# Performance work log

Measured on AMD Instinct MI355X. Metric: run time of the kernel, lower is better.

The kernel has to match this reference:

```python
import jax, jax.numpy as jnp
import numpy as np

V = 5023      # CoMA mesh vertices
K = 8         # avg neighbors per vertex
E = V * K     # edges
B = 64        # batch
C_IN = 3      # xyz
C_HID = 64    # conv width (layer_info)
M = 9         # kernel_size: number of weight matrices
LATENT = 128


def fsc_conv(x, src, dst, aw, u, c, W, b):
    """Feature-steered graph conv (translation invariant: v = -u).
    x: [B,V,C]; edge e: (i=src[e], j=dst[e]) with adjacency weight aw[e].
    y_i = b + sum_j a_ij * sum_m softmax_m(u_m.(x_i-x_j)+c_m) * (x_j @ W_m)
    """
    Bx, Vx, C = x.shape
    D = W.shape[2]
    xi = x[:, src]                                  # [B,E,C]
    xj = x[:, dst]                                  # [B,E,C]
    logits = jnp.einsum('bec,cm->bem', xi - xj, u) + c   # [B,E,M]
    att = jax.nn.softmax(logits, axis=-1) * aw[None, :, None]
    y = jnp.zeros((Bx, Vx, D), x.dtype)
    for m in range(W.shape[0]):                     # small fixed loop over M
        agg = jnp.zeros((Bx, Vx, C), x.dtype).at[:, src].add(att[:, :, m:m + 1] * xj)
        y = y + agg @ W[m]
    return y + b


def setup_inputs() -> dict:
    key = jax.random.key(0)
    ks = jax.random.split(key, 16)
    x = jax.random.normal(ks[0], (B, V, C_IN), jnp.float32)
    # mesh-like adjacency: each vertex i has K random neighbors, weight 1/K
    src = jnp.repeat(jnp.arange(V, dtype=jnp.int32), K)
    dst = jax.random.randint(ks[1], (E,), 0, V, dtype=jnp.int32)
    aw = jnp.full((E,), 1.0 / K, jnp.float32)
    g = lambda k, shp, fan: jax.random.normal(k, shp, jnp.float32) * np.float32(np.sqrt(2.0 / fan))
    # encoder conv params
    u_e = g(ks[2], (C_IN, M), C_IN + M)
    c_e = jnp.zeros((M,), jnp.float32)
    W_e = g(ks[3], (M, C_IN, C_HID), C_IN + C_HID)
    b_e = jnp.zeros((C_HID,), jnp.float32)
    # encoder latent dense: [V*C_HID, LATENT]
    W_enc = g(ks[4], (V * C_HID, LATENT), V * C_HID)
    b_enc = jnp.zeros((LATENT,), jnp.float32)
    # decoder latent dense: [LATENT, C_HID*V]
    W_dec = g(ks[5], (LATENT, C_HID * V), LATENT)
    b_dec = jnp.zeros((C_HID * V,), jnp.float32)
    # decoder conv params
    u_d = g(ks[6], (C_HID, M), C_HID + M)
    c_d = jnp.zeros((M,), jnp.float32)
    W_d = g(ks[7], (M, C_HID, C_IN), C_HID + C_IN)
    b_d = jnp.zeros((C_IN,), jnp.float32)
    return {'x': x, 'aw': aw, 'u_e': u_e, 'c_e': c_e, 'W_e': W_e, 'b_e': b_e,
            'W_enc': W_enc, 'b_enc': b_enc, 'W_dec': W_dec, 'b_dec': b_dec,
            'u_d': u_d, 'c_d': c_d, 'W_d': W_d, 'b_d': b_d,
            'src': src, 'dst': dst}


def reference(x, aw, u_e, c_e, W_e, b_e, W_enc, b_enc, W_dec, b_dec,
              u_d, c_d, W_d, b_d, src, dst):
    # Encoder: feature-steered conv -> relu -> flatten -> dense to latent
    h = jax.nn.relu(fsc_conv(x, src, dst, aw, u_e, c_e, W_e, b_e))   # [B,V,C_HID]
    z = h.reshape(h.shape[0], -1) @ W_enc + b_enc                    # [B,LATENT]
    # Decoder: dense -> reshape [B,V,C_HID] -> feature-steered conv -> relu
    d = (z @ W_dec + b_dec).reshape(z.shape[0], V, -1)               # [B,V,C_HID]
    out = jax.nn.relu(fsc_conv(d, src, dst, aw, u_d, c_d, W_d, b_d)) # [B,V,3]
    return out
```

## Files before the change

### kernel.cpp

```cpp
#include <hip/hip_runtime.h>

#define VN 5023
#define KN 8
#define BN 64
#define CIN 3
#define CH 64
#define MN 9
#define LAT 128
#define KTOT (VN*CH)
#define NBV (BN*VN)
#define KC 256
#define NCHUNK 1256
#define RED_G 8
#define RED_J 157
#define NXCD 8

__global__ __launch_bounds__(256, 4) void k_conv1(
    const float* __restrict__ x, const float* __restrict__ aw,
    const int* __restrict__ dst,
    const float* __restrict__ u_e, const float* __restrict__ c_e,
    const float* __restrict__ W_e, const float* __restrict__ b_e,
    float* __restrict__ h)
{
  int t = blockIdx.x*256 + threadIdx.x;
  if (t >= NBV) return;
  int b = t / VN, v = t - b*VN;
  const float* xb = x + (size_t)b*VN*CIN;
  int e0 = v*KN;
  int4 j01 = *(const int4*)(dst + e0);
  int4 j23 = *(const int4*)(dst + e0 + 4);
  int jj[8] = {j01.x,j01.y,j01.z,j01.w, j23.x,j23.y,j23.z,j23.w};
  float4 a01 = *(const float4*)(aw + e0);
  float4 a23 = *(const float4*)(aw + e0 + 4);
  float awv[8] = {a01.x,a01.y,a01.z,a01.w, a23.x,a23.y,a23.z,a23.w};
  float xj0[8], xj1[8], xj2[8];
#pragma unroll
  for (int k=0;k<KN;k++){
    const float* xr = xb + (size_t)jj[k]*3;
    xj0[k]=xr[0]; xj1[k]=xr[1]; xj2[k]=xr[2];
  }
  __builtin_amdgcn_sched_barrier(0);
  float xi0 = xb[v*3+0], xi1 = xb[v*3+1], xi2 = xb[v*3+2];
  float Ti[MN];
#pragma unroll
  for (int m=0;m<MN;m++)
    Ti[m] = xi0*u_e[m] + xi1*u_e[MN+m] + xi2*u_e[2*MN+m] + c_e[m];
  float agg[27];
#pragma unroll
  for (int i=0;i<27;i++) agg[i]=0.f;
#pragma unroll
  for (int k=0;k<KN;k++){
    float lg[MN];
#pragma unroll
    for (int m=0;m<MN;m++)
      lg[m] = Ti[m] - (xj0[k]*u_e[m]+xj1[k]*u_e[MN+m]+xj2[k]*u_e[2*MN+m]);
    float mx = lg[0];
#pragma unroll
    for (int m=1;m<MN;m++) mx = fmaxf(mx, lg[m]);
    float ex[MN], s=0.f;
#pragma unroll
    for (int m=0;m<MN;m++){ ex[m] = __expf(lg[m]-mx); s += ex[m]; }
    float r = awv[k] / s;
#pragma unroll
    for (int m=0;m<MN;m++){
      float a = ex[m]*r;
      agg[m*3+0] += a*xj0[k]; agg[m*3+1] += a*xj1[k]; agg[m*3+2] += a*xj2[k];
    }
  }
  float* hr = h + (size_t)t*CH;
  for (int cc=0; cc<4; cc++){
    float y[16];
#pragma unroll
    for (int c=0;c<16;c++) y[c] = b_e[cc*16+c];
#pragma unroll
    for (int mc=0; mc<27; mc++){
      float a = agg[mc];
#pragma unroll
      for (int c=0;c<16;c++) y[c] += a * W_e[mc*CH + cc*16 + c];
    }
#pragma unroll
    for (int c=0;c<16;c+=4){
      float4 o = make_float4(fmaxf(y[c],0.f),fmaxf(y[c+1],0.f),
                             fmaxf(y[c+2],0.f),fmaxf(y[c+3],0.f));
      *(float4*)(hr + cc*16 + c) = o;
    }
  }
}

__global__ __launch_bounds__(128, 4) void k_enc(
    const float* __restrict__ h, const float* __restrict__ We,
    float* __restrict__ partial)
{
  __shared__ float wlds[2][32*128];
  __shared__ float hlds[2][32][68];
  int t = threadIdx.x;
  int blk = blockIdx.x;
  int lq = t & 15;
  int bq = t >> 4;
  float acc[8][8];
#pragma unroll
  for (int i=0;i<8;i++)
#pragma unroll
    for (int j=0;j<8;j++) acc[i][j]=0.f;
  int kbase0 = blk*KC;
  int ldb = t & 63;
  int seg = t >> 6;
  int nt0 = (blk == NCHUNK-1) ? 6 : 8;

  float4 wreg[8], hreg[4];
  {
    const float* wsrc = We + (size_t)kbase0*LAT;
#pragma unroll
    for (int q=0;q<8;q++) wreg[q] = *(const float4*)(wsrc + (q*128+t)*4);
    const float* hsrc = h + (size_t)ldb*KTOT + kbase0 + seg*16;
#pragma unroll
    for (int q=0;q<4;q++) hreg[q] = *(const float4*)(hsrc + q*4);
#pragma unroll
    for (int q=0;q<8;q++) *(float4*)(&wlds[0][(q*128+t)*4]) = wreg[q];
#pragma unroll
    for (int q=0;q<4;q++){
      hlds[0][seg*16+q*4+0][ldb]=hreg[q].x; hlds[0][seg*16+q*4+1][ldb]=hreg[q].y;
      hlds[0][seg*16+q*4+2][ldb]=hreg[q].z; hlds[0][seg*16+q*4+3][ldb]=hreg[q].w;
    }
  }
  __syncthreads();

  int cur = 0;
  for (int t0=0; t0<nt0; t0++){
    bool pf = (t0+1 < nt0);
    if (pf){
      int kbase = kbase0 + (t0+1)*32;
      const float* wsrc = We + (size_t)kbase*LAT;
#pragma unroll
      for (int q=0;q<8;q++) wreg[q] = *(const float4*)(wsrc + (q*128+t)*4);
      const float* hsrc = h + (size_t)ldb*KTOT + kbase + seg*16;
#pragma unroll
      for (int q=0;q<4;q++) hreg[q] = *(const float4*)(hsrc + q*4);
    }
    __builtin_amdgcn_sched_barrier(0);
#pragma unroll 4
    for (int kk=0; kk<32; kk++){
      float4 w0 = *(const float4*)(&wlds[cur][kk*128 + lq*4]);
      float4 w1 = *(const float4*)(&wlds[cur][kk*128 + 64 + lq*4]);
      float4 z0 = *(const float4*)(&hlds[cur][kk][bq*8]);
      float4 z1 = *(const float4*)(&hlds[cur][kk][bq*8+4]);
      float wv[8] = {w0.x,w0.y,w0.z,w0.w,w1.x,w1.y,w1.z,w1.w};
      float zv[8] = {z0.x,z0.y,z0.z,z0.w,z1.x,z1.y,z1.z,z1.w};
#pragma unroll
      for (int li=0;li<8;li++)
#pragma unroll
        for (int bi=0;bi<8;bi++) acc[li][bi] += wv[li]*zv[bi];
    }
    if (pf){
      int nb = cur^1;
#pragma unroll
      for (int q=0;q<8;q++) *(float4*)(&wlds[nb][(q*128+t)*4]) = wreg[q];
#pragma unroll
      for (int q=0;q<4;q++){
        hlds[nb][seg*16+q*4+0][ldb]=hreg[q].x; hlds[nb][seg*16+q*4+1][ldb]=hreg[q].y;
        hlds[nb][seg*16+q*4+2][ldb]=hreg[q].z; hlds[nb][seg*16+q*4+3][ldb]=hreg[q].w;
      }
    }
    __syncthreads();
    cur ^= 1;
  }
  float* pp = partial + (size_t)blk*(BN*LAT);
#pragma unroll
  for (int bi=0;bi<8;bi++){
    int b = bq*8+bi;
    float4 o0 = make_float4(acc[0][bi],acc[1][bi],acc[2][bi],acc[3][bi]);
    float4 o1 = make_float4(acc[4][bi],acc[5][bi],acc[6][bi],acc[7][bi]);
    *(float4*)(pp + b*LAT + lq*4)      = o0;
    *(float4*)(pp + b*LAT + 64 + lq*4) = o1;
  }
}

__global__ __launch_bounds__(256) void k_red1(
    const float* __restrict__ partial, float* __restrict__ partial2)
{
  int idx = blockIdx.x*256 + threadIdx.x;
  int g = blockIdx.y;
  float s = 0.f;
  for (int j=0;j<RED_J;j++)
    s += partial[(size_t)(g + RED_G*j)*(BN*LAT) + idx];
  partial2[(size_t)g*(BN*LAT) + idx] = s;
}

__global__ __launch_bounds__(256) void k_red2(
    const float* __restrict__ partial2, const float* __restrict__ b_enc,
    float* __restrict__ zT)
{
  int idx = blockIdx.x*256 + threadIdx.x;
  float s = 0.f;
#pragma unroll
  for (int g=0; g<RED_G; g++) s += partial2[(size_t)g*(BN*LAT) + idx];
  int b = idx >> 7, l = idx & 127;
  zT[l*BN + b] = s + b_enc[l];
}

__global__ __launch_bounds__(256, 8) void k_dectg(
    const float* __restrict__ zT, const float* __restrict__ Wd,
    const float* __restrict__ b_dec, const float* __restrict__ u_d,
    const float* __restrict__ W_d, float* __restrict__ TG)
{
  __shared__ float4 dt4[4][512];
  int t = threadIdx.x;
  int lane = t & 63;
  int wv = __builtin_amdgcn_readfirstlane(t >> 6);
  int blk = blockIdx.x;
  int vc = blk*256 + lane*4;
  int vs = vc < (KTOT-4) ? vc : (KTOT-4);
  const float* wp = Wd + vs;
  const float* zrow = zT + wv*16;
  float acc[4][16];
#pragma unroll
  for (int i=0;i<4;i++)
#pragma unroll
    for (int j=0;j<16;j++) acc[i][j]=0.f;

  float4 wA[4], wB[4];
#pragma unroll
  for (int u=0;u<4;u++) wA[u] = *(const float4*)(wp + (size_t)u*KTOT);

  for (int l0=0; l0<LAT; l0+=8){
#pragma unroll
    for (int u=0;u<4;u++) wB[u] = *(const float4*)(wp + (size_t)(l0+4+u)*KTOT);
    __builtin_amdgcn_sched_barrier(0);
#pragma unroll
    for (int u=0;u<4;u++){
      int l = l0+u;
      float zv[16];
#pragma unroll
      for (int j=0;j<16;j++) zv[j] = zrow[l*BN + j];
      float wvv[4] = {wA[u].x,wA[u].y,wA[u].z,wA[u].w};
#pragma unroll
      for (int i=0;i<4;i++)
#pragma unroll
        for (int j=0;j<16;j++) acc[i][j] += wvv[i]*zv[j];
    }
    if (l0+8 < LAT){
#pragma unroll
      for (int u=0;u<4;u++) wA[u] = *(const float4*)(wp + (size_t)(l0+8+u)*KTOT);
    }
    __builtin_amdgcn_sched_barrier(0);
#pragma unroll
    for (int u=0;u<4;u++){
      int l = l0+4+u;
      float zv[16];
#pragma unroll
      for (int j=0;j<16;j++) zv[j] = zrow[l*BN + j];
      float wvv[4] = {wB[u].x,wB[u].y,wB[u].z,wB[u].w};
#pragma unroll
      for (int i=0;i<4;i++)
#pragma unroll
        for (int j=0;j<16;j++) acc[i][j] += wvv[i]*zv[j];
    }
  }
  float4 bd = *(const float4*)(b_dec + vs);
  float bdv[4] = {bd.x, bd.y, bd.z, bd.w};
  int chb = lane & 15;
  int vl4 = lane >> 4;

#pragma unroll
  for (int hh=0; hh<2; hh++){
#pragma unroll
    for (int jj=0; jj<8; jj++){
      int j = hh*8 + jj;
      dt4[wv][vl4*128 + jj*16 + (chb^jj)] =
        make_float4(acc[0][j]+bdv[0], acc[1][j]+bdv[1],
                    acc[2][j]+bdv[2], acc[3][j]+bdv[3]);
    }
    __syncthreads();
    if (lane < 32){
      int vl = lane >> 3, bl = lane & 7;
      int vg = blk*4 + vl;
      if (vg < VN){
        float Tg[36];
#pragma unroll
        for (int q=0;q<36;q++) Tg[q]=0.f;
#pragma unroll 1
        for (int cb=0; cb<16; cb++){
          float4 dq = dt4[wv][vl*128 + bl*16 + (cb^bl)];
          float dv4[4] = {dq.x,dq.y,dq.z,dq.w};
#pragma unroll
          for (int ii=0; ii<4; ii++){
            int c = cb*4 + ii;
            float dv = dv4[ii];
            const float* ur = u_d + c*MN;
#pragma unroll
            for (int m=0;m<MN;m++) Tg[m] += dv*ur[m];
#pragma unroll
            for (int m=0;m<MN;m++){
              const float* wr = W_d + (m*CH + c)*3;
              Tg[9+m*3+0] += dv*wr[0];
              Tg[9+m*3+1] += dv*wr[1];
              Tg[9+m*3+2] += dv*wr[2];
            }
          }
        }
        int bg = wv*16 + hh*8 + bl;
        float* tg = TG + (size_t)((size_t)bg*VN + vg)*36;
#pragma unroll
        for (int q=0;q<9;q++)
          *(float4*)(tg + q*4) = make_float4(Tg[q*4+0],Tg[q*4+1],
                                             Tg[q*4+2],Tg[q*4+3]);
      }
    }
    __syncthreads();
  }
}

__global__ __launch_bounds__(256, 4) void k_att(
    const float* __restrict__ TG, const float* __restrict__ aw,
    const int* __restrict__ dst, const float* __restrict__ c_d,
    const float* __restrict__ b_d, float* __restrict__ out)
{
  int wg = blockIdx.x;
  int wgid = (wg & 7)*157 + (wg >> 3);
  int t = wgid*256 + threadIdx.x;
  if (t >= NBV) return;
  int b = t / VN, v = t - b*VN;
  const float* TGb = TG + (size_t)b*VN*36;
  int e0 = v*KN;
  int4 j01 = *(const int4*)(dst + e0);
  int4 j23 = *(const int4*)(dst + e0 + 4);
  int jj[8] = {j01.x,j01.y,j01.z,j01.w, j23.x,j23.y,j23.z,j23.w};
  float4 a01 = *(const float4*)(aw + e0);
  float4 a23 = *(const float4*)(aw + e0 + 4);
  float awv[8] = {a01.x,a01.y,a01.z,a01.w, a23.x,a23.y,a23.z,a23.w};
  float Ti[MN];
#pragma unroll
  for (int m=0;m<MN;m++) Ti[m] = TGb[(size_t)v*36+m] + c_d[m];
  float y0=0.f, y1=0.f, y2=0.f;
  float4 q[9];
  {
    const float* Rp = TGb + (size_t)jj[0]*36;
#pragma unroll
    for (int i=0;i<9;i++) q[i] = *(const float4*)(Rp + i*4);
  }
#pragma unroll
  for (int k=0;k<KN;k++){
    float4 p[9];
    if (k+1 < KN){
      const float* Rp = TGb + (size_t)jj[k+1]*36;
#pragma unroll
      for (int i=0;i<9;i++) p[i] = *(const float4*)(Rp + i*4);
    }
    float rr[36] = {q[0].x,q[0].y,q[0].z,q[0].w, q[1].x,q[1].y,q[1].z,q[1].w,
                    q[2].x,q[2].y,q[2].z,q[2].w, q[3].x,q[3].y,q[3].z,q[3].w,
                    q[4].x,q[4].y,q[4].z,q[4].w, q[5].x,q[5].y,q[5].z,q[5].w,
                    q[6].x,q[6].y,q[6].z,q[6].w, q[7].x,q[7].y,q[7].z,q[7].w,
                    q[8].x,q[8].y,q[8].z,q[8].w};
    float lg[MN];
#pragma unroll
    for (int m=0;m<MN;m++) lg[m] = Ti[m] - rr[m];
    float mx = lg[0];
#pragma unroll
    for (int m=1;m<MN;m++) mx = fmaxf(mx, lg[m]);
    float ex[MN], s=0.f;
#pragma unroll
    for (int m=0;m<MN;m++){ ex[m] = __expf(lg[m]-mx); s += ex[m]; }
    float sc = awv[k] / s;
#pragma unroll
    for (int m=0;m<MN;m++){
      float a = ex[m]*sc;
      y0 += a*rr[9+m*3+0]; y1 += a*rr[9+m*3+1]; y2 += a*rr[9+m*3+2];
    }
    if (k+1 < KN){
#pragma unroll
      for (int i=0;i<9;i++) q[i] = p[i];
    }
  }
  float* o = out + (size_t)t*3;
  o[0]=fmaxf(y0+b_d[0],0.f); o[1]=fmaxf(y1+b_d[1],0.f); o[2]=fmaxf(y2+b_d[2],0.f);
}

extern "C" void kernel_launch(void* const* d_in, const int* in_sizes, int n_in,
                              void* d_out, int out_size, void* d_ws, size_t ws_size,
                              hipStream_t stream) {
  const float* x     = (const float*)d_in[0];
  const float* aw    = (const float*)d_in[1];
  const float* u_e   = (const float*)d_in[2];
  const float* c_e   = (const float*)d_in[3];
  const float* W_e   = (const float*)d_in[4];
  const float* b_e   = (const float*)d_in[5];
  const float* W_enc = (const float*)d_in[6];
  const float* b_enc = (const float*)d_in[7];
  const float* W_dec = (const float*)d_in[8];
  const float* b_dec = (const float*)d_in[9];
  const float* u_d   = (const float*)d_in[10];
  const float* c_d   = (const float*)d_in[11];
  const float* W_d   = (const float*)d_in[12];
  const float* b_d   = (const float*)d_in[13];
  const int*   dst   = (const int*)d_in[15];
  float* out = (float*)d_out;

  char* ws = (char*)d_ws;
  float* hbuf = (float*)ws;
  float* zT   = (float*)ws;
  float* partial2 = (float*)(ws + (64<<10));
  size_t off1 = (size_t)NBV*CH*sizeof(float);
  float* partial = (float*)(ws + off1);
  float* TGbuf   = (float*)(ws + off1);

  int grid_bv = (NBV + 255)/256;

  k_conv1<<<grid_bv,256,0,stream>>>(x, aw, dst, u_e, c_e, W_e, b_e, hbuf);
  k_enc<<<NCHUNK,128,0,stream>>>(hbuf, W_enc, partial);
  dim3 gr1(32, RED_G);
  k_red1<<<gr1,256,0,stream>>>(partial, partial2);
  k_red2<<<32,256,0,stream>>>(partial2, b_enc, zT);
  int grid_dec = (KTOT + 255)/256;
  k_dectg<<<grid_dec,256,0,stream>>>(zT, W_dec, b_dec, u_d, W_d, TGbuf);
  k_att<<<grid_bv,256,0,stream>>>(TGbuf, aw, dst, c_d, b_d, out);
}
```

Before: 353.9 us.

## Fuse encoder graph conv into latent GEMM, keeping activations in LDS

Merges the first feature-steered conv kernel with the encoder dense-layer split-K GEMM. Each block now computes h for its 4 vertices across all 64 batches directly into a 64KB shared tile, so the 82MB h tensor is never written to or read from global memory. The GEMM switches to 256 threads with a single-buffered weight tile and extra barriers, and occupancy drops to 2 blocks per SM because of the larger LDS footprint. The conv work is also redistributed per block, which may worsen latency hiding for the gathers.

Result: faster. 327.3 us (-7.5%).

```diff
diff --git a/kernel.cpp b/kernel.cpp
--- a/kernel.cpp
+++ b/kernel.cpp
@@ -15,159 +15,133 @@
 #define RED_J 157
 #define NXCD 8
 
-__global__ __launch_bounds__(256, 4) void k_conv1(
+__global__ __launch_bounds__(256, 2) void k_convenc(
     const float* __restrict__ x, const float* __restrict__ aw,
     const int* __restrict__ dst,
     const float* __restrict__ u_e, const float* __restrict__ c_e,
     const float* __restrict__ W_e, const float* __restrict__ b_e,
-    float* __restrict__ h)
-{
-  int t = blockIdx.x*256 + threadIdx.x;
-  if (t >= NBV) return;
-  int b = t / VN, v = t - b*VN;
-  const float* xb = x + (size_t)b*VN*CIN;
-  int e0 = v*KN;
-  int4 j01 = *(const int4*)(dst + e0);
-  int4 j23 = *(const int4*)(dst + e0 + 4);
-  int jj[8] = {j01.x,j01.y,j01.z,j01.w, j23.x,j23.y,j23.z,j23.w};
-  float4 a01 = *(const float4*)(aw + e0);
-  float4 a23 = *(const float4*)(aw + e0 + 4);
-  float awv[8] = {a01.x,a01.y,a01.z,a01.w, a23.x,a23.y,a23.z,a23.w};
-  float xj0[8], xj1[8], xj2[8];
-#pragma unroll
-  for (int k=0;k<KN;k++){
-    const float* xr = xb + (size_t)jj[k]*3;
-    xj0[k]=xr[0]; xj1[k]=xr[1]; xj2[k]=xr[2];
-  }
-  __builtin_amdgcn_sched_barrier(0);
-  float xi0 = xb[v*3+0], xi1 = xb[v*3+1], xi2 = xb[v*3+2];
-  float Ti[MN];
-#pragma unroll
-  for (int m=0;m<MN;m++)
-    Ti[m] = xi0*u_e[m] + xi1*u_e[MN+m] + xi2*u_e[2*MN+m] + c_e[m];
-  float agg[27];
-#pragma unroll
-  for (int i=0;i<27;i++) agg[i]=0.f;
-#pragma unroll
-  for (int k=0;k<KN;k++){
-    float lg[MN];
-#pragma unroll
-    for (int m=0;m<MN;m++)
-      lg[m] = Ti[m] - (xj0[k]*u_e[m]+xj1[k]*u_e[MN+m]+xj2[k]*u_e[2*MN+m]);
-    float mx = lg[0];
-#pragma unroll
-    for (int m=1;m<MN;m++) mx = fmaxf(mx, lg[m]);
-    float ex[MN], s=0.f;
-#pragma unroll
-    for (int m=0;m<MN;m++){ ex[m] = __expf(lg[m]-mx); s += ex[m]; }
-    float r = awv[k] / s;
-#pragma unroll
-    for (int m=0;m<MN;m++){
-      float a = ex[m]*r;
-      agg[m*3+0] += a*xj0[k]; agg[m*3+1] += a*xj1[k]; agg[m*3+2] += a*xj2[k];
-    }
-  }
-  float* hr = h + (size_t)t*CH;
-  for (int cc=0; cc<4; cc++){
-    float y[16];
-#pragma unroll
-    for (int c=0;c<16;c++) y[c] = b_e[cc*16+c];
-#pragma unroll
-    for (int mc=0; mc<27; mc++){
-      float a = agg[mc];
-#pragma unroll
-      for (int c=0;c<16;c++) y[c] += a * W_e[mc*CH + cc*16 + c];
-    }
-#pragma unroll
-    for (int c=0;c<16;c+=4){
-      float4 o = make_float4(fmaxf(y[c],0.f),fmaxf(y[c+1],0.f),
-                             fmaxf(y[c+2],0.f),fmaxf(y[c+3],0.f));
-      *(float4*)(hr + cc*16 + c) = o;
-    }
-  }
-}
-
-__global__ __launch_bounds__(128, 4) void k_enc(
-    const float* __restrict__ h, const float* __restrict__ We,
-    float* __restrict__ partial)
-{
-  __shared__ float wlds[2][32*128];
-  __shared__ float hlds[2][32][68];
+    const float* __restrict__ We, float* __restrict__ partial)
+{
+  __shared__ float wlds[32*128];
+  __shared__ float htile[256*64];
   int t = threadIdx.x;
   int blk = blockIdx.x;
+  int lane = t & 63;
+  int vl = __builtin_amdgcn_readfirstlane(t >> 6);
+  int vg = blk*4 + vl;
+  int kbase0 = blk*KC;
+
+  float4 wreg[4];
+  {
+    const float* wsrc = We + (size_t)kbase0*LAT;
+#pragma unroll
+    for (int q=0;q<4;q++) wreg[q] = *(const float4*)(wsrc + (q*256+t)*4);
+  }
+
+  if (vg < VN){
+    int e0 = vg*KN;
+    int jj[KN]; float awv[KN];
+#pragma unroll
+    for (int k=0;k<KN;k++){ jj[k] = dst[e0+k]; awv[k] = aw[e0+k]; }
+    const float* xb = x + (size_t)lane*VN*CIN;
+    float xj0[KN], xj1[KN], xj2[KN];
+#pragma unroll
+    for (int k=0;k<KN;k++){
+      const float* xr = xb + (size_t)jj[k]*3;
+      xj0[k]=xr[0]; xj1[k]=xr[1]; xj2[k]=xr[2];
+    }
+    __builtin_amdgcn_sched_barrier(0);
+    float xi0 = xb[(size_t)vg*3+0], xi1 = xb[(size_t)vg*3+1],
+          xi2 = xb[(size_t)vg*3+2];
+    float Ti[MN];
+#pragma unroll
+    for (int m=0;m<MN;m++)
+      Ti[m] = xi0*u_e[m] + xi1*u_e[MN+m] + xi2*u_e[2*MN+m] + c_e[m];
+    float agg[27];
+#pragma unroll
+    for (int i=0;i<27;i++) agg[i]=0.f;
+#pragma unroll
+    for (int k=0;k<KN;k++){
+      float lg[MN];
+#pragma unroll
+      for (int m=0;m<MN;m++)
+        lg[m] = Ti[m] - (xj0[k]*u_e[m]+xj1[k]*u_e[MN+m]+xj2[k]*u_e[2*MN+m]);
+      float mx = lg[0];
+#pragma unroll
+      for (int m=1;m<MN;m++) mx = fmaxf(mx, lg[m]);
+      float ex[MN], s=0.f;
+#pragma unroll
+      for (int m=0;m<MN;m++){ ex[m] = __expf(lg[m]-mx); s += ex[m]; }
+      float r = awv[k] / s;
+#pragma unroll
+      for (int m=0;m<MN;m++){
+        float a = ex[m]*r;
+        agg[m*3+0] += a*xj0[k]; agg[m*3+1] += a*xj1[k]; agg[m*3+2] += a*xj2[k];
+      }
+    }
+    for (int cc=0; cc<4; cc++){
+      float y[16];
+#pragma unroll
+      for (int c=0;c<16;c++) y[c] = b_e[cc*16+c];
+#pragma unroll
+      for (int mc=0; mc<27; mc++){
+        float a = agg[mc];
+#pragma unroll
+        for (int c=0;c<16;c++) y[c] += a * W_e[mc*CH + cc*16 + c];
+      }
+#pragma unroll
+      for (int c=0;c<16;c++)
+        htile[(vl*64 + cc*16 + c)*64 + lane] = fmaxf(y[c], 0.f);
+    }
+  } else {
+#pragma unroll
+    for (int c=0;c<CH;c++) htile[(vl*64+c)*64 + lane] = 0.f;
+  }
+
+#pragma unroll
+  for (int q=0;q<4;q++) *(float4*)(&wlds[(q*256+t)*4]) = wreg[q];
+  __syncthreads();
+
   int lq = t & 15;
   int bq = t >> 4;
-  float acc[8][8];
+  float acc[8][4];
 #pragma unroll
   for (int i=0;i<8;i++)
 #pragma unroll
-    for (int j=0;j<8;j++) acc[i][j]=0.f;
-  int kbase0 = blk*KC;
-  int ldb = t & 63;
-  int seg = t >> 6;
+    for (int j=0;j<4;j++) acc[i][j]=0.f;
   int nt0 = (blk == NCHUNK-1) ? 6 : 8;
 
-  float4 wreg[8], hreg[4];
-  {
-    const float* wsrc = We + (size_t)kbase0*LAT;
-#pragma unroll
-    for (int q=0;q<8;q++) wreg[q] = *(const float4*)(wsrc + (q*128+t)*4);
-    const float* hsrc = h + (size_t)ldb*KTOT + kbase0 + seg*16;
-#pragma unroll
-    for (int q=0;q<4;q++) hreg[q] = *(const float4*)(hsrc + q*4);
-#pragma unroll
-    for (int q=0;q<8;q++) *(float4*)(&wlds[0][(q*128+t)*4]) = wreg[q];
-#pragma unroll
-    for (int q=0;q<4;q++){
-      hlds[0][seg*16+q*4+0][ldb]=hreg[q].x; hlds[0][seg*16+q*4+1][ldb]=hreg[q].y;
-      hlds[0][seg*16+q*4+2][ldb]=hreg[q].z; hlds[0][seg*16+q*4+3][ldb]=hreg[q].w;
-    }
-  }
-  __syncthreads();
-
-  int cur = 0;
   for (int t0=0; t0<nt0; t0++){
     bool pf = (t0+1 < nt0);
     if (pf){
-      int kbase = kbase0 + (t0+1)*32;
-      const float* wsrc = We + (size_t)kbase*LAT;
-#pragma unroll
-      for (int q=0;q<8;q++) wreg[q] = *(const float4*)(wsrc + (q*128+t)*4);
-      const float* hsrc = h + (size_t)ldb*KTOT + kbase + seg*16;
-#pragma unroll
-      for (int q=0;q<4;q++) hreg[q] = *(const float4*)(hsrc + q*4);
+      const float* wsrc = We + (size_t)(kbase0 + (t0+1)*32)*LAT;
+#pragma unroll
+      for (int q=0;q<4;q++) wreg[q] = *(const float4*)(wsrc + (q*256+t)*4);
     }
     __builtin_amdgcn_sched_barrier(0);
 #pragma unroll 4
     for (int kk=0; kk<32; kk++){
-      float4 w0 = *(const float4*)(&wlds[cur][kk*128 + lq*4]);
-      float4 w1 = *(const float4*)(&wlds[cur][kk*128 + 64 + lq*4]);
-      float4 z0 = *(const float4*)(&hlds[cur][kk][bq*8]);
-      float4 z1 = *(const float4*)(&hlds[cur][kk][bq*8+4]);
+      float4 w0 = *(const float4*)(&wlds[kk*128 + lq*4]);
+      float4 w1 = *(const float4*)(&wlds[kk*128 + 64 + lq*4]);
+      float4 z  = *(const float4*)(&htile[(t0*32+kk)*64 + bq*4]);
       float wv[8] = {w0.x,w0.y,w0.z,w0.w,w1.x,w1.y,w1.z,w1.w};
-      float zv[8] = {z0.x,z0.y,z0.z,z0.w,z1.x,z1.y,z1.z,z1.w};
+      float zv[4] = {z.x,z.y,z.z,z.w};
 #pragma unroll
       for (int li=0;li<8;li++)
 #pragma unroll
-        for (int bi=0;bi<8;bi++) acc[li][bi] += wv[li]*zv[bi];
-    }
+        for (int bi=0;bi<4;bi++) acc[li][bi] += wv[li]*zv[bi];
+    }
+    __syncthreads();
     if (pf){
-      int nb = cur^1;
-#pragma unroll
-      for (int q=0;q<8;q++) *(float4*)(&wlds[nb][(q*128+t)*4]) = wreg[q];
-#pragma unroll
-      for (int q=0;q<4;q++){
-        hlds[nb][seg*16+q*4+0][ldb]=hreg[q].x; hlds[nb][seg*16+q*4+1][ldb]=hreg[q].y;
-        hlds[nb][seg*16+q*4+2][ldb]=hreg[q].z; hlds[nb][seg*16+q*4+3][ldb]=hreg[q].w;
-      }
-    }
-    __syncthreads();
-    cur ^= 1;
+#pragma unroll
+      for (int q=0;q<4;q++) *(float4*)(&wlds[(q*256+t)*4]) = wreg[q];
+      __syncthreads();
+    }
   }
   float* pp = partial + (size_t)blk*(BN*LAT);
 #pragma unroll
-  for (int bi=0;bi<8;bi++){
-    int b = bq*8+bi;
+  for (int bi=0;bi<4;bi++){
+    int b = bq*4+bi;
     float4 o0 = make_float4(acc[0][bi],acc[1][bi],acc[2][bi],acc[3][bi]);
     float4 o1 = make_float4(acc[4][bi],acc[5][bi],acc[6][bi],acc[7][bi]);
     *(float4*)(pp + b*LAT + lq*4)      = o0;
@@ -396,7 +370,6 @@
   float* out = (float*)d_out;
 
   char* ws = (char*)d_ws;
-  float* hbuf = (float*)ws;
   float* zT   = (float*)ws;
   float* partial2 = (float*)(ws + (64<<10));
   size_t off1 = (size_t)NBV*CH*sizeof(float);
@@ -405,8 +378,8 @@
 
   int grid_bv = (NBV + 255)/256;
 
-  k_conv1<<<grid_bv,256,0,stream>>>(x, aw, dst, u_e, c_e, W_e, b_e, hbuf);
-  k_enc<<<NCHUNK,128,0,stream>>>(hbuf, W_enc, partial);
+  k_convenc<<<NCHUNK,256,0,stream>>>(x, aw, dst, u_e, c_e, W_e, b_e,
+                                     W_enc, partial);
   dim3 gr1(32, RED_G);
   k_red1<<<gr1,256,0,stream>>>(partial, partial2);
   k_red2<<<32,256,0,stream>>>(partial2, b_enc, zT);
```
